# Kernel optimization log

Measured on AMD Instinct MI355X. Metric: run time of the kernel, lower is better.

The kernel has to match this reference:

```python
import jax, jax.numpy as jnp
import numpy as np

DIM = 128
WH, WW = 8, 8
N = WH * WW            # tokens per window = 64
H = 8                  # num_heads
HD = DIM // H          # head_dim = 16
SCALE = HD ** -0.5
B = 2                  # true batch
NW = 1024              # windows per image (256x256 / 8x8)
B_ = B * NW            # 2048 windows total
NFT = 2                # num_frame_type
TABLE = (2 * WH - 1) * (2 * WW - 1)  # 225


def _relative_position_index():
    coords = np.stack(np.meshgrid(np.arange(WH), np.arange(WW), indexing='ij'))  # (2, WH, WW)
    cf = coords.reshape(2, -1)                        # (2, N)
    rel = cf[:, :, None] - cf[:, None, :]             # (2, N, N)
    rel = rel.transpose(1, 2, 0).astype(np.int64)     # (N, N, 2)
    rel[..., 0] += WH - 1
    rel[..., 1] += WW - 1
    rel[..., 0] *= 2 * WW - 1
    return rel.sum(-1)                                # (N, N) in [0, 224]


def setup_inputs() -> dict:
    key = jax.random.key(0)
    ks = jax.random.split(key, 12)
    x = jax.random.normal(ks[0], (B_, N, DIM), dtype=jnp.float32)
    # 0 / -100 additive window mask (shifted-window pattern surrogate)
    mask = jnp.where(jax.random.uniform(ks[1], (NW, N, N)) > 0.9, -100.0, 0.0).astype(jnp.float32)
    frame_type = jax.random.uniform(ks[2], (B, NFT), dtype=jnp.float32)
    qkv_w = jax.random.normal(ks[3], (3 * DIM, DIM), dtype=jnp.float32) * 0.02
    qkv_b = jnp.zeros((3 * DIM,), dtype=jnp.float32)
    table = jax.random.normal(ks[4], (TABLE, H), dtype=jnp.float32) * 0.02
    proj_w = jax.random.normal(ks[5], (DIM, DIM), dtype=jnp.float32) * 0.02
    proj_b = jnp.zeros((DIM,), dtype=jnp.float32)
    aff_w1 = jax.random.normal(ks[6], (16, NFT), dtype=jnp.float32) * 0.1
    aff_b1 = jnp.zeros((16,), dtype=jnp.float32)
    aff_w2 = jax.random.normal(ks[7], (2 * DIM, 16), dtype=jnp.float32) * 0.1
    rel_index = jnp.asarray(_relative_position_index(), dtype=jnp.int32)
    return {"x": x, "mask": mask, "frame_type": frame_type,
            "qkv_w": qkv_w, "qkv_b": qkv_b, "table": table,
            "proj_w": proj_w, "proj_b": proj_b,
            "aff_w1": aff_w1, "aff_b1": aff_b1, "aff_w2": aff_w2,
            "rel_index": rel_index}


def reference(x, mask, frame_type, qkv_w, qkv_b, table, proj_w, proj_b,
              aff_w1, aff_b1, aff_w2, rel_index):
    # qkv projection: (B_, N, 3C) -> (3, B_, H, N, HD)
    qkv = (x @ qkv_w.T + qkv_b).reshape(B_, N, 3, H, HD).transpose(2, 0, 3, 1, 4)
    q, k, v = qkv[0], qkv[1], qkv[2]
    attn = jnp.einsum('bhnd,bhmd->bhnm', q * SCALE, k)          # (B_, H, N, N)
    rpb = table[rel_index].transpose(2, 0, 1)                    # (H, N, N)
    attn = attn + rpb[None]
    # add window mask: (B, NW, H, N, N)
    attn = attn.reshape(B_ // NW, NW, H, N, N) + mask[None, :, None]
    attn = jax.nn.softmax(attn.reshape(B_, H, N, N), axis=-1)
    # FA affine modulation of V
    hdn = jax.nn.sigmoid(frame_type @ aff_w1.T + aff_b1)         # (B, 16)
    ap = hdn @ aff_w2.T                                          # (B, 2C)
    scale_p, bias_p = jnp.split(ap, 2, axis=-1)                  # each (B, C)
    scale_p = jnp.repeat(scale_p, B_ // B, axis=0).reshape(B_, H, 1, HD)
    bias_p = jnp.repeat(bias_p, B_ // B, axis=0).reshape(B_, H, 1, HD)
    v = jax.nn.softplus(scale_p) * v + bias_p
    out = jnp.einsum('bhnm,bhmd->bhnd', attn, v)                 # (B_, H, N, HD)
    out = out.transpose(0, 2, 1, 3).reshape(B_, N, DIM)
    return out @ proj_w.T + proj_b
```

## Files before the change

### kernel.cpp

```cpp
#include <hip/hip_runtime.h>
#include <hip/hip_bf16.h>

#define NWIN 2048
#define LOG2E 1.44269504f
#define QSCALE 0.36067376f

#define OFF_AFF 0
#define OFF_RPB 512
#define OFF_WQ  33280
#define OFF_WP  57856

typedef __attribute__((ext_vector_type(8))) __bf16 bf16x8;
typedef __attribute__((ext_vector_type(4))) float floatx4;
typedef __attribute__((ext_vector_type(4))) short short4v;

#if __has_builtin(__builtin_amdgcn_exp2f)
#define EXP2F __builtin_amdgcn_exp2f
#else
#define EXP2F exp2f
#endif

__global__ __launch_bounds__(256) void prep_kernel(
    const float* __restrict__ frame_type, const float* __restrict__ qkv_w,
    const float* __restrict__ table, const float* __restrict__ proj_w,
    const float* __restrict__ aff_w1, const float* __restrict__ aff_b1,
    const float* __restrict__ aff_w2, const int* __restrict__ rel_index,
    float* __restrict__ ws)
{
  const int gid = blockIdx.x * 256 + threadIdx.x;
  if (gid < 49152) {
    int j = gid & 7, lane = (gid >> 3) & 63, kt = (gid >> 9) & 3, nt = gid >> 11;
    int n = nt * 16 + (lane & 15);
    int k = kt * 32 + (lane >> 4) * 8 + j;
    ((__bf16*)(ws + OFF_WQ))[gid] = (__bf16)qkv_w[n * 128 + k];
  }
  if (gid < 16384) {
    int j = gid & 3, lane = (gid >> 2) & 63, nt = (gid >> 8) & 7, h = gid >> 11;
    int n = nt * 16 + (lane & 15);
    int k = h * 16 + (lane >> 4) * 4 + j;
    ((__bf16*)(ws + OFF_WP))[gid] = (__bf16)proj_w[n * 128 + k];
  }
  if (gid < 32768) {
    int h = gid >> 12, rem = gid & 4095;
    ws[OFF_RPB + gid] = table[rel_index[rem] * 8 + h] * LOG2E;
  }
  if (gid < 512) {
    int b = gid >> 8, c2 = gid & 255;
    float hd[16];
    #pragma unroll
    for (int j = 0; j < 16; ++j) {
      float t = frame_type[b*2+0]*aff_w1[j*2+0] + frame_type[b*2+1]*aff_w1[j*2+1] + aff_b1[j];
      hd[j] = 1.0f / (1.0f + expf(-t));
    }
    float ap = 0.f;
    #pragma unroll
    for (int j = 0; j < 16; ++j) ap += hd[j] * aff_w2[c2*16 + j];
    float r = (c2 < 128) ? ((ap > 20.f) ? ap : log1pf(expf(ap))) : ap;
    ws[OFF_AFF + gid] = r;
  }
}

__global__ __launch_bounds__(256, 3) void attn_kernel(
    const float* __restrict__ x, const float* __restrict__ mask,
    const float* __restrict__ qkv_b, const float* __restrict__ proj_b,
    const float* __restrict__ ws, float* __restrict__ out)
{
  __shared__ __attribute__((aligned(16))) __bf16 sK [64 * 128];
  __shared__ __attribute__((aligned(16))) __bf16 sVT[128 * 64];

#define SKI(row, col) ((row)*128 + ((col) ^ (((row)&3)<<4) ^ ((row)&4)))
#define SVI(ch, tok)  ((ch)*64  + ((tok) ^ (((ch)&7)<<3)))
#define SBAR() __builtin_amdgcn_sched_barrier(0)

  const int w    = blockIdx.x;
  const int b    = w >> 10;
  const int tid  = threadIdx.x;
  const int wv   = tid >> 6;
  const int lane = tid & 63;
  const int quad = lane >> 4;
  const int l15  = lane & 15;
  const int row0 = wv * 16;

  bf16x8 af[4][4];
  {
    const float* xw = x + (size_t)w * 8192;
    #pragma unroll
    for (int mt = 0; mt < 4; ++mt)
      #pragma unroll
      for (int kt = 0; kt < 4; ++kt) {
        const float* p = xw + (mt*16 + l15) * 128 + kt*32 + quad*8;
        float4 f0 = *(const float4*)p;
        float4 f1 = *(const float4*)(p + 4);
        bf16x8 v;
        v[0]=(__bf16)f0.x; v[1]=(__bf16)f0.y; v[2]=(__bf16)f0.z; v[3]=(__bf16)f0.w;
        v[4]=(__bf16)f1.x; v[5]=(__bf16)f1.y; v[6]=(__bf16)f1.z; v[7]=(__bf16)f1.w;
        af[mt][kt] = v;
      }
  }

  const __bf16* wq = (const __bf16*)(ws + OFF_WQ);

  {
    #pragma unroll
    for (int t = 0; t < 4; ++t) {
      const int nt = 8 + ((t >> 1) << 3) + ((t & 1) << 2) + wv;
      bf16x8 bfr[4];
      #pragma unroll
      for (int kt = 0; kt < 4; ++kt)
        bfr[kt] = *(const bf16x8*)(wq + ((size_t)(nt*4 + kt) * 64 + lane) * 8);
      const float bias = qkv_b[nt*16 + l15];
      const int col = nt*16 + l15;
      #pragma unroll
      for (int mt = 0; mt < 4; ++mt) {
        floatx4 acc = {bias, bias, bias, bias};
        #pragma unroll
        for (int kt = 0; kt < 4; ++kt)
          acc = __builtin_amdgcn_mfma_f32_16x16x32_bf16(af[mt][kt], bfr[kt], acc, 0, 0, 0);
        if (nt < 16) {
          const int c = col - 128;
          const int srow0 = ((((quad & 1) << 1) + (mt >> 1)) << 4)
                          + ((((mt & 1) << 1) | (quad >> 1)) << 2);
          #pragma unroll
          for (int r = 0; r < 4; ++r) sK[SKI(srow0 + r, c)] = (__bf16)acc[r];
        } else {
          const int c = col - 256;
          const float sp = ws[OFF_AFF + b*256 + c];
          const float bp = ws[OFF_AFF + b*256 + 128 + c];
          const int rowb = mt*16 + quad*4;
          #pragma unroll
          for (int r = 0; r < 4; ++r) sVT[SVI(c, rowb + r)] = (__bf16)fmaf(sp, acc[r], bp);
        }
      }
    }
  }

  bf16x8 aq[4];
  #pragma unroll
  for (int kt = 0; kt < 4; ++kt) aq[kt] = af[0][kt];
  #pragma unroll
  for (int mt = 1; mt < 4; ++mt)
    if (wv == mt) {
      #pragma unroll
      for (int kt = 0; kt < 4; ++kt) aq[kt] = af[mt][kt];
    }

  short4v qa[8];
  {
    #pragma unroll
    for (int nt = 0; nt < 8; ++nt) {
      bf16x8 bfr[4];
      #pragma unroll
      for (int kt = 0; kt < 4; ++kt)
        bfr[kt] = *(const bf16x8*)(wq + ((size_t)(nt*4 + kt) * 64 + lane) * 8);
      floatx4 acc = *(const floatx4*)(qkv_b + nt*16 + quad*4);
      #pragma unroll
      for (int kt = 0; kt < 4; ++kt)
        acc = __builtin_amdgcn_mfma_f32_16x16x32_bf16(bfr[kt], aq[kt], acc, 0, 0, 0);
      union { short4v s; __bf16 h4[4]; } u;
      #pragma unroll
      for (int r = 0; r < 4; ++r) u.h4[r] = (__bf16)(acc[r] * QSCALE);
      qa[nt] = u.s;
    }
  }
  __syncthreads();

  floatx4 mv[4];
  {
    const float* mrow = mask + (size_t)(w & 1023) * 4096 + (row0 + l15) * 64;
    #pragma unroll
    for (int jt = 0; jt < 4; ++jt) {
      const int joff = ((jt & 1) << 5) + ((jt >> 1) << 2) + (quad << 3);
      floatx4 m4 = *(const floatx4*)(mrow + joff);
      #pragma unroll
      for (int r = 0; r < 4; ++r) mv[jt][r] = m4[r] * LOG2E;
    }
  }

  floatx4 pacc[8];
  #pragma unroll
  for (int nt = 0; nt < 8; ++nt) {
    float pb = proj_b[nt*16 + l15];
    pacc[nt] = (floatx4){pb, pb, pb, pb};
  }

  bf16x8 ones;
  #pragma unroll
  for (int i = 0; i < 8; ++i) ones[i] = (__bf16)1.0f;

  const float* rpb = ws + OFF_RPB;
  const __bf16* wp = (const __bf16*)(ws + OFF_WP);

#define HLOAD(H, RQ, KB) do {                                               \
    _Pragma("unroll")                                                       \
    for (int jt = 0; jt < 4; ++jt) {                                        \
      const int joff = ((jt & 1) << 5) + ((jt >> 1) << 2) + (quad << 3);    \
      RQ[jt] = *(const floatx4*)(rpb + (H)*4096 + (row0 + l15)*64 + joff);  \
      KB[jt] = *(const short4v*)(&sK[SKI(jt*16 + l15, (H)*16 + quad*4)]);   \
    }                                                                       \
  } while (0)

#define HCOMP(H, RQ, KB) do {                                               \
    short4v wpf[8];                                                         \
    _Pragma("unroll")                                                       \
    for (int nt = 0; nt < 8; ++nt)                                          \
      wpf[nt] = *(const short4v*)(wp + ((size_t)((H)*8 + nt)*64 + lane)*4); \
    floatx4 s_[4];                                                          \
    _Pragma("unroll")                                                       \
    for (int jt = 0; jt < 4; ++jt) {                                        \
      floatx4 ci = RQ[jt] + mv[jt];                                         \
      s_[jt] = __builtin_amdgcn_mfma_f32_16x16x16bf16_1k(KB[jt], qa[H], ci, 0, 0, 0); \
    }                                                                       \
    union { bf16x8 v; __bf16 e[8]; } p0, p1;                                \
    _Pragma("unroll")                                                       \
    for (int r = 0; r < 4; ++r) {                                           \
      p0.e[r]     = (__bf16)EXP2F(s_[0][r]);                                \
      p0.e[4 + r] = (__bf16)EXP2F(s_[2][r]);                                \
      p1.e[r]     = (__bf16)EXP2F(s_[1][r]);                                \
      p1.e[4 + r] = (__bf16)EXP2F(s_[3][r]);                                \
    }                                                                       \
    bf16x8 vb0 = *(const bf16x8*)(&sVT[SVI((H)*16 + l15, quad*8)]);         \
    bf16x8 vb1 = *(const bf16x8*)(&sVT[SVI((H)*16 + l15, 32 + quad*8)]);    \
    floatx4 o2 = {0.f,0.f,0.f,0.f}, sm_ = {0.f,0.f,0.f,0.f};                \
    o2  = __builtin_amdgcn_mfma_f32_16x16x32_bf16(vb0, p0.v, o2, 0, 0, 0);  \
    sm_ = __builtin_amdgcn_mfma_f32_16x16x32_bf16(ones, p0.v, sm_, 0, 0, 0);\
    o2  = __builtin_amdgcn_mfma_f32_16x16x32_bf16(vb1, p1.v, o2, 0, 0, 0);  \
    sm_ = __builtin_amdgcn_mfma_f32_16x16x32_bf16(ones, p1.v, sm_, 0, 0, 0);\
    const float inv = 1.0f / sm_[0];                                        \
    union { short4v s; __bf16 hh_[4]; } u_;                                 \
    _Pragma("unroll")                                                       \
    for (int r = 0; r < 4; ++r) u_.hh_[r] = (__bf16)(o2[r] * inv);          \
    _Pragma("unroll")                                                       \
    for (int nt = 0; nt < 8; ++nt)                                          \
      pacc[nt] = __builtin_amdgcn_mfma_f32_16x16x16bf16_1k(u_.s, wpf[nt], pacc[nt], 0, 0, 0); \
  } while (0)

  {
    floatx4 rqA[4], rqB[4];
    short4v kbA[4], kbB[4];
    HLOAD(0, rqA, kbA);
    #pragma unroll 1
    for (int hh = 0; hh < 4; ++hh) {
      const int h0 = hh * 2;
      SBAR();
      HLOAD(h0 + 1, rqB, kbB);
      SBAR();
      HCOMP(h0, rqA, kbA);
      SBAR();
      if (hh < 3) HLOAD(h0 + 2, rqA, kbA);
      SBAR();
      HCOMP(h0 + 1, rqB, kbB);
    }
  }
#undef HLOAD
#undef HCOMP

  {
    float* ow = out + (size_t)w * 8192;
    #pragma unroll
    for (int nt = 0; nt < 8; ++nt)
      #pragma unroll
      for (int r = 0; r < 4; ++r)
        ow[(row0 + quad*4 + r)*128 + nt*16 + l15] = pacc[nt][r];
  }
#undef SKI
#undef SVI
#undef SBAR
}

extern "C" void kernel_launch(void* const* d_in, const int* in_sizes, int n_in,
                              void* d_out, int out_size, void* d_ws, size_t ws_size,
                              hipStream_t stream)
{
  const float* x          = (const float*)d_in[0];
  const float* mask       = (const float*)d_in[1];
  const float* frame_type = (const float*)d_in[2];
  const float* qkv_w      = (const float*)d_in[3];
  const float* qkv_b      = (const float*)d_in[4];
  const float* table      = (const float*)d_in[5];
  const float* proj_w     = (const float*)d_in[6];
  const float* proj_b     = (const float*)d_in[7];
  const float* aff_w1     = (const float*)d_in[8];
  const float* aff_b1     = (const float*)d_in[9];
  const float* aff_w2     = (const float*)d_in[10];
  const int*   rel_index  = (const int*)d_in[11];
  float* ws   = (float*)d_ws;
  float* outp = (float*)d_out;

  prep_kernel<<<192, 256, 0, stream>>>(frame_type, qkv_w, table, proj_w,
                                       aff_w1, aff_b1, aff_w2, rel_index, ws);
  attn_kernel<<<NWIN, 256, 0, stream>>>(x, mask, qkv_b, proj_b, ws, outp);
}
```

Measured before the change: 223.9 us.

## Split per-head attention and projection into two fully unrolled phases

Replaces the manually software-pipelined loop over heads (with sched_barriers and double-buffered loads) with a fully unrolled first phase that computes the attention output for all eight heads into registers. A second phase then runs the output projection MFMAs. This frees the compiler to interleave loads and MFMAs across heads and keeps the pacc accumulators out of the live range during the attention phase. It also swaps the division for a hardware reciprocal. The risks are the loss of explicit scheduling control and higher register pressure from the unrolled code under the 3-blocks-per-CU launch bound.

```diff
diff --git a/kernel.cpp b/kernel.cpp
--- a/kernel.cpp
+++ b/kernel.cpp
@@ -18,6 +18,11 @@
 #define EXP2F __builtin_amdgcn_exp2f
 #else
 #define EXP2F exp2f
+#endif
+#if __has_builtin(__builtin_amdgcn_rcpf)
+#define RCPF __builtin_amdgcn_rcpf
+#else
+#define RCPF(x) (1.0f / (x))
 #endif
 
 __global__ __launch_bounds__(256) void prep_kernel(
@@ -70,7 +75,6 @@
 
 #define SKI(row, col) ((row)*128 + ((col) ^ (((row)&3)<<4) ^ ((row)&4)))
 #define SVI(ch, tok)  ((ch)*64  + ((tok) ^ (((ch)&7)<<3)))
-#define SBAR() __builtin_amdgcn_sched_barrier(0)
 
   const int w    = blockIdx.x;
   const int b    = w >> 10;
@@ -176,13 +180,6 @@
     }
   }
 
-  floatx4 pacc[8];
-  #pragma unroll
-  for (int nt = 0; nt < 8; ++nt) {
-    float pb = proj_b[nt*16 + l15];
-    pacc[nt] = (floatx4){pb, pb, pb, pb};
-  }
-
   bf16x8 ones;
   #pragma unroll
   for (int i = 0; i < 8; ++i) ones[i] = (__bf16)1.0f;
@@ -190,69 +187,68 @@
   const float* rpb = ws + OFF_RPB;
   const __bf16* wp = (const __bf16*)(ws + OFF_WP);
 
-#define HLOAD(H, RQ, KB) do {                                               \
+#define PHASEA(H, U) do {                                                   \
+    floatx4 rq_[4];                                                         \
+    short4v kb_[4];                                                         \
     _Pragma("unroll")                                                       \
     for (int jt = 0; jt < 4; ++jt) {                                        \
       const int joff = ((jt & 1) << 5) + ((jt >> 1) << 2) + (quad << 3);    \
-      RQ[jt] = *(const floatx4*)(rpb + (H)*4096 + (row0 + l15)*64 + joff);  \
-      KB[jt] = *(const short4v*)(&sK[SKI(jt*16 + l15, (H)*16 + quad*4)]);   \
+      rq_[jt] = *(const floatx4*)(rpb + (H)*4096 + (row0 + l15)*64 + joff); \
+      kb_[jt] = *(const short4v*)(&sK[SKI(jt*16 + l15, (H)*16 + quad*4)]);  \
     }                                                                       \
-  } while (0)
-
-#define HCOMP(H, RQ, KB) do {                                               \
-    short4v wpf[8];                                                         \
-    _Pragma("unroll")                                                       \
-    for (int nt = 0; nt < 8; ++nt)                                          \
-      wpf[nt] = *(const short4v*)(wp + ((size_t)((H)*8 + nt)*64 + lane)*4); \
     floatx4 s_[4];                                                          \
     _Pragma("unroll")                                                       \
     for (int jt = 0; jt < 4; ++jt) {                                        \
-      floatx4 ci = RQ[jt] + mv[jt];                                         \
-      s_[jt] = __builtin_amdgcn_mfma_f32_16x16x16bf16_1k(KB[jt], qa[H], ci, 0, 0, 0); \
+      floatx4 ci = rq_[jt] + mv[jt];                                        \
+      s_[jt] = __builtin_amdgcn_mfma_f32_16x16x16bf16_1k(kb_[jt], qa[H], ci, 0, 0, 0); \
     }                                                                       \
-    union { bf16x8 v; __bf16 e[8]; } p0, p1;                                \
+    union { bf16x8 v; __bf16 e[8]; } p0_, p1_;                              \
     _Pragma("unroll")                                                       \
     for (int r = 0; r < 4; ++r) {                                           \
-      p0.e[r]     = (__bf16)EXP2F(s_[0][r]);                                \
-      p0.e[4 + r] = (__bf16)EXP2F(s_[2][r]);                                \
-      p1.e[r]     = (__bf16)EXP2F(s_[1][r]);                                \
-      p1.e[4 + r] = (__bf16)EXP2F(s_[3][r]);                                \
+      p0_.e[r]     = (__bf16)EXP2F(s_[0][r]);                               \
+      p0_.e[4 + r] = (__bf16)EXP2F(s_[2][r]);                               \
+      p1_.e[r]     = (__bf16)EXP2F(s_[1][r]);                               \
+      p1_.e[4 + r] = (__bf16)EXP2F(s_[3][r]);                               \
     }                                                                       \
     bf16x8 vb0 = *(const bf16x8*)(&sVT[SVI((H)*16 + l15, quad*8)]);         \
     bf16x8 vb1 = *(const bf16x8*)(&sVT[SVI((H)*16 + l15, 32 + quad*8)]);    \
     floatx4 o2 = {0.f,0.f,0.f,0.f}, sm_ = {0.f,0.f,0.f,0.f};                \
-    o2  = __builtin_amdgcn_mfma_f32_16x16x32_bf16(vb0, p0.v, o2, 0, 0, 0);  \
-    sm_ = __builtin_amdgcn_mfma_f32_16x16x32_bf16(ones, p0.v, sm_, 0, 0, 0);\
-    o2  = __builtin_amdgcn_mfma_f32_16x16x32_bf16(vb1, p1.v, o2, 0, 0, 0);  \
-    sm_ = __builtin_amdgcn_mfma_f32_16x16x32_bf16(ones, p1.v, sm_, 0, 0, 0);\
-    const float inv = 1.0f / sm_[0];                                        \
+    o2  = __builtin_amdgcn_mfma_f32_16x16x32_bf16(vb0, p0_.v, o2, 0, 0, 0); \
+    sm_ = __builtin_amdgcn_mfma_f32_16x16x32_bf16(ones, p0_.v, sm_, 0, 0, 0);\
+    o2  = __builtin_amdgcn_mfma_f32_16x16x32_bf16(vb1, p1_.v, o2, 0, 0, 0); \
+    sm_ = __builtin_amdgcn_mfma_f32_16x16x32_bf16(ones, p1_.v, sm_, 0, 0, 0);\
+    const float inv = RCPF(sm_[0]);                                         \
     union { short4v s; __bf16 hh_[4]; } u_;                                 \
     _Pragma("unroll")                                                       \
     for (int r = 0; r < 4; ++r) u_.hh_[r] = (__bf16)(o2[r] * inv);          \
+    U = u_.s;                                                               \
+  } while (0)
+
+  short4v u0, u1, u2, u3, u4, u5, u6, u7;
+  PHASEA(0, u0); PHASEA(1, u1); PHASEA(2, u2); PHASEA(3, u3);
+  PHASEA(4, u4); PHASEA(5, u5); PHASEA(6, u6); PHASEA(7, u7);
+#undef PHASEA
+
+  floatx4 pacc[8];
+  #pragma unroll
+  for (int nt = 0; nt < 8; ++nt) {
+    float pb = proj_b[nt*16 + l15];
+    pacc[nt] = (floatx4){pb, pb, pb, pb};
+  }
+
+#define PHASEB(H, U) do {                                                   \
+    short4v wpf_[8];                                                        \
     _Pragma("unroll")                                                       \
     for (int nt = 0; nt < 8; ++nt)                                          \
-      pacc[nt] = __builtin_amdgcn_mfma_f32_16x16x16bf16_1k(u_.s, wpf[nt], pacc[nt], 0, 0, 0); \
+      wpf_[nt] = *(const short4v*)(wp + ((size_t)((H)*8 + nt)*64 + lane)*4);\
+    _Pragma("unroll")                                                       \
+    for (int nt = 0; nt < 8; ++nt)                                          \
+      pacc[nt] = __builtin_amdgcn_mfma_f32_16x16x16bf16_1k(U, wpf_[nt], pacc[nt], 0, 0, 0); \
   } while (0)
 
-  {
-    floatx4 rqA[4], rqB[4];
-    short4v kbA[4], kbB[4];
-    HLOAD(0, rqA, kbA);
-    #pragma unroll 1
-    for (int hh = 0; hh < 4; ++hh) {
-      const int h0 = hh * 2;
-      SBAR();
-      HLOAD(h0 + 1, rqB, kbB);
-      SBAR();
-      HCOMP(h0, rqA, kbA);
-      SBAR();
-      if (hh < 3) HLOAD(h0 + 2, rqA, kbA);
-      SBAR();
-      HCOMP(h0 + 1, rqB, kbB);
-    }
-  }
-#undef HLOAD
-#undef HCOMP
+  PHASEB(0, u0); PHASEB(1, u1); PHASEB(2, u2); PHASEB(3, u3);
+  PHASEB(4, u4); PHASEB(5, u5); PHASEB(6, u6); PHASEB(7, u7);
+#undef PHASEB
 
   {
     float* ow = out + (size_t)w * 8192;
@@ -264,7 +260,6 @@
   }
 #undef SKI
 #undef SVI
-#undef SBAR
 }
 
 extern "C" void kernel_launch(void* const* d_in, const int* in_sizes, int n_in,
```

After: 218.6 us. 1.02x faster.
